# Optimization experiments

Measured on AMD Instinct MI355X. Metric: run time of the kernel, lower is better.

Reference implementation:

```python
import jax, jax.numpy as jnp
import numpy as np
from jax import lax

T, B = 64, 16
N, W, R = 256, 64, 4          # mem_slot, mem_size, read_heads
IN, OUT = 64, 64
NHID, NNOUT = 256, 256
IF_SIZE = W * R + 3 * W + 5 * R + 3  # 471
EPS = 1e-6


def setup_inputs() -> dict:
    key = jax.random.key(0)
    ks = jax.random.split(key, 8)
    in_dim = IN + R * W
    def glorot(k, shape):
        fan_in = shape[0]
        return jax.random.normal(k, shape, dtype=jnp.float32) / np.sqrt(fan_in)
    return {
        "input_data": jax.random.normal(ks[0], (T, B, IN), dtype=jnp.float32),
        "W1": glorot(ks[1], (in_dim, NHID)),
        "b1": jnp.zeros((NHID,), jnp.float32),
        "W2": glorot(ks[2], (NHID, NNOUT)),
        "b2": jnp.zeros((NNOUT,), jnp.float32),
        "W_if": glorot(ks[3], (NNOUT, IF_SIZE)),
        "b_if": jnp.zeros((IF_SIZE,), jnp.float32),
        "W_out": glorot(ks[4], (NNOUT, OUT)),
        "W_mem_out": glorot(ks[5], (R * W, OUT)),
    }


def oneplus(x):
    return 1.0 + jax.nn.softplus(x)


def content_address(mem, keys, strengths):
    # mem [B,N,W], keys [B,W,R], strengths [B,R] -> weights [B,N,R]
    mem_n = mem / (jnp.linalg.norm(mem, axis=-1, keepdims=True) + EPS)
    key_n = keys / (jnp.linalg.norm(keys, axis=1, keepdims=True) + EPS)
    sim = jnp.einsum('bnw,bwr->bnr', mem_n, key_n)
    return jax.nn.softmax(sim * strengths[:, None, :], axis=1)


def parse_interface(z):
    # z: [B, IF_SIZE] -> dict of interface components (NeuCom layout)
    o = 0
    read_keys = z[:, o:o + W * R].reshape(-1, W, R); o += W * R
    read_str = oneplus(z[:, o:o + R]); o += R
    write_key = z[:, o:o + W]; o += W
    write_str = oneplus(z[:, o:o + 1]); o += 1
    erase = jax.nn.sigmoid(z[:, o:o + W]); o += W
    write_vec = z[:, o:o + W]; o += W
    free_gates = jax.nn.sigmoid(z[:, o:o + R]); o += R
    alloc_gate = jax.nn.sigmoid(z[:, o:o + 1]); o += 1
    write_gate = jax.nn.sigmoid(z[:, o:o + 1]); o += 1
    read_modes = jax.nn.softmax(z[:, o:o + 3 * R].reshape(-1, 3, R), axis=1)
    return (read_keys, read_str, write_key, write_str, erase, write_vec,
            free_gates, alloc_gate, write_gate, read_modes)


def _dnc_forward(input_data, W1, b1, W2, b2, W_if, b_if, W_out, W_mem_out):
    Bz = input_data.shape[1]
    eye = jnp.eye(N, dtype=input_data.dtype)

    def step(carry, x_t):
        mem, usage, rw, ww, prec, link, rvec = carry
        # --- controller (feedforward) ---
        ctrl_in = jnp.concatenate([x_t, rvec.reshape(Bz, R * W)], axis=1)
        h = jnp.tanh(ctrl_in @ W1 + b1)
        nn_out = jnp.tanh(h @ W2 + b2)
        (read_keys, read_str, write_key, write_str, erase, write_vec,
         free_gates, alloc_gate, write_gate, read_modes) = parse_interface(nn_out @ W_if + b_if)
        # --- write ---
        retention = jnp.prod(1.0 - free_gates[:, None, :] * rw, axis=2)   # [B,N]
        usage = (usage + ww - usage * ww) * retention
        idx = jnp.argsort(usage, axis=1)                                  # ascending usage
        u_sorted = jnp.take_along_axis(usage, idx, axis=1)
        prod_excl = jnp.concatenate(
            [jnp.ones((Bz, 1), usage.dtype), jnp.cumprod(u_sorted, axis=1)[:, :-1]], axis=1)
        alloc_sorted = (1.0 - u_sorted) * prod_excl
        alloc = jnp.take_along_axis(alloc_sorted, jnp.argsort(idx, axis=1), axis=1)
        wc = content_address(mem, write_key[:, :, None], write_str)[:, :, 0]  # [B,N]
        ww = write_gate * (alloc_gate * alloc + (1.0 - alloc_gate) * wc)
        mem = mem * (1.0 - ww[:, :, None] * erase[:, None, :]) \
              + ww[:, :, None] * write_vec[:, None, :]
        link = (1.0 - ww[:, :, None] - ww[:, None, :]) * link \
               + ww[:, :, None] * prec[:, None, :]
        link = link * (1.0 - eye)
        prec = (1.0 - jnp.sum(ww, axis=1, keepdims=True)) * prec + ww
        # --- read ---
        rc = content_address(mem, read_keys, read_str)                    # [B,N,R]
        fwd_w = jnp.einsum('bnm,bmr->bnr', link, rw)
        bwd_w = jnp.einsum('bmn,bmr->bnr', link, rw)
        rw = (bwd_w * read_modes[:, 0][:, None, :]
              + rc * read_modes[:, 1][:, None, :]
              + fwd_w * read_modes[:, 2][:, None, :])
        rvec = jnp.einsum('bnw,bnr->bwr', mem, rw)                        # [B,W,R]
        out = nn_out @ W_out + rvec.reshape(Bz, R * W) @ W_mem_out
        view = (free_gates, alloc_gate, write_gate, rw, ww, usage)
        return (mem, usage, rw, ww, prec, link, rvec), (out, view)

    carry0 = (
        jnp.full((Bz, N, W), EPS, input_data.dtype),   # mem_mat
        jnp.zeros((Bz, N), input_data.dtype),          # usage
        jnp.zeros((Bz, N, R), input_data.dtype),       # read_weight
        jnp.zeros((Bz, N), input_data.dtype),          # write_weight
        jnp.zeros((Bz, N), input_data.dtype),          # precedence
        jnp.zeros((Bz, N, N), input_data.dtype),       # link matrix
        jnp.zeros((Bz, W, R), input_data.dtype),       # read vectors
    )
    _, (outputs, _view) = lax.scan(step, carry0, input_data)
    return outputs  # [T,B,OUT]


def reference(input_data, W1, b1, W2, b2, W_if, b_if, W_out, W_mem_out):
    return _dnc_forward(input_data, W1, b1, W2, b2, W_if, b_if, W_out, W_mem_out)
```

## Files before the change

kernel.cpp:

```cpp
#include <hip/hip_runtime.h>
#include <hip/hip_fp16.h>
#include <math.h>

#define Tt 64
#define Bb 16
#define Nn 256
#define Ww 64
#define Rr 4
#define INd 64
#define OUTd 64
#define IFS 471
#define EPSf 1e-6f

#define W1OFF   0
#define W2OFF   40960
#define WIFOFF  73728
#define WOUTOFF 134016
#define WMEMOFF 142208
#define WTOT    150400

#define LROW    129
#define LINKB   (256 * LROW * 4)
#define SCRB    16384
#define FIXF    3456
#define SMEM_MAIN (LINKB + SCRB + FIXF * 4)
#define SMEM_FB   (SCRB + FIXF * 4)

#define RWS 132

typedef _Float16 h2v __attribute__((ext_vector_type(2)));
__device__ __forceinline__ float fdot2(__half2 a, __half2 b, float c) {
    return __builtin_amdgcn_fdot2(*(h2v*)&a, *(h2v*)&b, c, false);
}
__device__ __forceinline__ __half2 pkh(float a, float b) {
    auto r = __builtin_amdgcn_cvt_pkrtz(a, b);
    return *(__half2*)&r;
}

__device__ __forceinline__ float sigm(float x) { return 1.f / (1.f + expf(-x)); }
__device__ __forceinline__ float oneplus_(float x) {
    return 1.f + fmaxf(x, 0.f) + log1pf(expf(-fabsf(x)));
}
__device__ __forceinline__ float wsum(float v) {
#pragma unroll
    for (int o = 32; o; o >>= 1) v += __shfl_xor(v, o, 64);
    return v;
}
__device__ __forceinline__ float wmaxr(float v) {
#pragma unroll
    for (int o = 32; o; o >>= 1) v = fmaxf(v, __shfl_xor(v, o, 64));
    return v;
}

__device__ __attribute__((noinline)) float gemv_part(
    const __half2* __restrict__ wP, int str, int iters,
    const __half2* __restrict__ vin)
{
    float a[8] = {0.f,0.f,0.f,0.f,0.f,0.f,0.f,0.f};
    float4 h0 = *(const float4*)(wP);
    float4 h1 = *(const float4*)(wP + str);
#pragma unroll 1
    for (int j0 = 0; j0 < iters - 8; j0 += 8) {
        int k8n = (j0 >> 2) + 2;
        float4 n0 = *(const float4*)(wP + (size_t)k8n * str);
        float4 n1 = *(const float4*)(wP + (size_t)(k8n + 1) * str);
        float4 v0 = *(const float4*)(vin + j0);
        float4 v1 = *(const float4*)(vin + j0 + 4);
        const __half2* hh0 = (const __half2*)&h0;
        const __half2* hh1 = (const __half2*)&h1;
        const __half2* vv0 = (const __half2*)&v0;
        const __half2* vv1 = (const __half2*)&v1;
#pragma unroll
        for (int u = 0; u < 4; ++u) a[u]     = fdot2(hh0[u], vv0[u], a[u]);
#pragma unroll
        for (int u = 0; u < 4; ++u) a[4 + u] = fdot2(hh1[u], vv1[u], a[4 + u]);
        h0 = n0; h1 = n1;
    }
    {
        float4 v0 = *(const float4*)(vin + iters - 8);
        float4 v1 = *(const float4*)(vin + iters - 4);
        const __half2* hh0 = (const __half2*)&h0;
        const __half2* hh1 = (const __half2*)&h1;
        const __half2* vv0 = (const __half2*)&v0;
        const __half2* vv1 = (const __half2*)&v1;
#pragma unroll
        for (int u = 0; u < 4; ++u) a[u]     = fdot2(hh0[u], vv0[u], a[u]);
#pragma unroll
        for (int u = 0; u < 4; ++u) a[4 + u] = fdot2(hh1[u], vv1[u], a[4 + u]);
    }
    return ((a[0]+a[1])+(a[2]+a[3])) + ((a[4]+a[5])+(a[6]+a[7]));
}

__global__ void convert_weights(const float* __restrict__ W1, const float* __restrict__ W2,
                                const float* __restrict__ Wif, const float* __restrict__ Wout,
                                const float* __restrict__ Wmem, __half2* __restrict__ wp) {
    int i = blockIdx.x * blockDim.x + threadIdx.x;
    if (i >= WTOT) return;
    float a, b;
    if (i < W2OFF) {
        int q = i & 3, s = i >> 2, n = s & 255, k2 = (s >> 8) * 4 + q;
        a = W1[(2*k2)*256+n];  b = W1[(2*k2+1)*256+n];
    } else if (i < WIFOFF) {
        int t = i - W2OFF;
        int q = t & 3, s = t >> 2, n = s & 255, k2 = (s >> 8) * 4 + q;
        a = W2[(2*k2)*256+n];  b = W2[(2*k2+1)*256+n];
    } else if (i < WOUTOFF) {
        int t = i - WIFOFF;
        int q = t & 3, s = t >> 2, o = s % IFS, k2 = (s / IFS) * 4 + q;
        a = Wif[(2*k2)*IFS+o]; b = Wif[(2*k2+1)*IFS+o];
    } else if (i < WMEMOFF) {
        int t = i - WOUTOFF;
        int q = t & 3, s = t >> 2, n = s & 63, k2 = (s >> 6) * 4 + q;
        a = Wout[(2*k2)*64+n]; b = Wout[(2*k2+1)*64+n];
    } else {
        int t = i - WMEMOFF;
        int q = t & 3, s = t >> 2, n = s & 63, k2 = (s >> 6) * 4 + q;
        a = Wmem[(2*k2)*64+n]; b = Wmem[(2*k2+1)*64+n];
    }
    wp[i] = __floats2half2_rn(a, b);
}

template <bool LLINK>
__global__ __launch_bounds__(1024) void dnc_kernel(
    const float* __restrict__ x, const float* __restrict__ b1,
    const float* __restrict__ b2, const float* __restrict__ bif,
    const __half2* __restrict__ wp,
    __half* __restrict__ memg,
    __half2* __restrict__ memWg,
    __half2* __restrict__ linkg,
    float* __restrict__ out)
{
    extern __shared__ __align__(16) char smem[];
    const int b = blockIdx.x;
    const int tid = threadIdx.x;
    const int lane = tid & 63;
    const int wv = tid >> 6;

    __half2* l2p = (__half2*)smem;
    __half2* gl2 = linkg + (size_t)b * (256 * LROW);
    float* scr   = (float*)(smem + (LLINK ? LINKB : 0));
    __half* scrh = (__half*)scr;
    float* fx    = (float*)((char*)scr + SCRB);

    float*   s_rw    = fx + 0;
    __half2* s_ctrlh = (__half2*)(fx + 1024);
    __half2* s_hh    = (__half2*)(fx + 1184);
    __half2* s_nnh   = (__half2*)(fx + 1312);
    __half2* s_rwh   = (__half2*)(fx + 1440);
    float* s_z     = fx + 1968;
    float* s_usage = fx + 2440;
    float* s_ww    = fx + 2696;
    float* s_prec  = fx + 2952;
    float* s_knorm = fx + 3208;
    float* s_rstr  = fx + 3212;
    float* s_rmode = fx + 3216;
    float* s_sc    = fx + 3228;
    float* s_red   = fx + 3232;
    float* s_er    = fx + 3264;
    __half2* s_keyh = (__half2*)(fx + 3328);
    float* s_srt   = scr + 1024;
    float* s_cp    = scr + 1280;
    __half2* s_keyw2 = (__half2*)(scr + 1280);
    float* s_wcdot = scr + 1536;
    float* s_wcss  = scr + 1792;
    __half2* s_wwh2 = (__half2*)(scr + 2048);
    __half2* s_tmh2 = (__half2*)(scr + 2304);

    __half*  memh  = memg + (size_t)b * (Ww * Nn);
    __half2* memh2 = (__half2*)memh;
    __half2* memW2 = memWg + (size_t)b * (32 * 256);
    __half*  memWh = (__half*)memW2;

    auto lread = [&](int idx) -> __half2 {
        if constexpr (LLINK) return l2p[idx]; else return gl2[idx];
    };
    auto lwrite = [&](int idx, __half2 v) {
        if constexpr (LLINK) l2p[idx] = v; else gl2[idx] = v;
    };

    {
        __half2 z2 = pkh(0.f, 0.f);
#pragma unroll 1
        for (int i = tid; i < 256 * LROW; i += 1024) lwrite(i, z2);
        __half2 e2 = __floats2half2_rn(EPSf, EPSf);
#pragma unroll 1
        for (int j = 0; j < 8; ++j) { memh2[tid + j * 1024] = e2; memW2[tid + j * 1024] = e2; }
        if (tid < 528) s_rwh[tid] = z2;
        if (tid < 32) {
            float2 xv = *(const float2*)&x[b * INd + 2 * tid];
            s_ctrlh[tid] = pkh(xv.x, xv.y);
        } else if (tid < 160) s_ctrlh[tid] = z2;
    }
    if (tid < 256) {
        s_usage[tid] = 0.f; s_ww[tid] = 0.f; s_prec[tid] = 0.f;
        s_rw[tid*4+0] = 0.f; s_rw[tid*4+1] = 0.f; s_rw[tid*4+2] = 0.f; s_rw[tid*4+3] = 0.f;
    }

#pragma unroll 1
    for (int t = 0; t < Tt; ++t) {
        __syncthreads();

        {
            int kc = wv >> 2, o = (wv & 3) * 64 + lane;
            scr[kc * 256 + o] = gemv_part(wp + W1OFF + o * 4 + kc * 10240, 1024, 40,
                                          s_ctrlh + kc * 40);
        }
        __syncthreads();
        if (tid < 256) {
            float v = tanhf(b1[tid] + ((scr[tid] + scr[256+tid]) + (scr[512+tid] + scr[768+tid])));
            float pv = __shfl_xor(v, 1, 64);
            if ((tid & 1) == 0) s_hh[tid >> 1] = pkh(v, pv);
        }
        __syncthreads();

        {
            int kc = wv >> 2, o = (wv & 3) * 64 + lane;
            scr[kc * 256 + o] = gemv_part(wp + W2OFF + o * 4 + kc * 8192, 1024, 32,
                                          s_hh + kc * 32);
        }
        __syncthreads();
        if (tid < 256) {
            float v = tanhf(b2[tid] + ((scr[tid] + scr[256+tid]) + (scr[512+tid] + scr[768+tid])));
            float pv = __shfl_xor(v, 1, 64);
            if ((tid & 1) == 0) s_nnh[tid >> 1] = pkh(v, pv);
        }
        __syncthreads();

        {
            int kc = wv >> 3, o = (wv & 7) * 64 + lane;
            if (o < IFS)
                scr[kc * 512 + o] = gemv_part(wp + WIFOFF + o * 4 + kc * 30144, 1884, 64,
                                              s_nnh + kc * 64);
        }
        __syncthreads();
        if (tid < IFS) {
            float v = bif[tid] + scr[tid] + scr[512 + tid];
            s_z[tid] = v;
            float pv1 = __shfl_xor(v, 1, 64);
            float pv4 = __shfl_xor(v, 4, 64);
            if (tid < 256) {
                if ((tid & 4) == 0)
                    s_keyh[(tid & 3) * 32 + (tid >> 3)] = pkh(v, pv4);
            } else if (tid >= 260 && tid < 324) {
                if ((tid & 1) == 0)
                    s_keyw2[(tid - 260) >> 1] = pkh(v, pv1);
            }
        }
        __syncthreads();

        if (wv < 4) {
            float vz = s_z[lane * 4 + wv];
            float s = wsum(vz * vz);
            if (lane == 0) s_knorm[wv] = sqrtf(s) + EPSf;
        } else if (wv == 4) {
            float vz = s_z[260 + lane];
            float s = wsum(vz * vz);
            if (lane == 0) s_sc[3] = sqrtf(s) + EPSf;
        } else if (wv == 5) {
            if (lane < 4) s_rstr[lane] = oneplus_(s_z[256 + lane]);
            else if (lane >= 8 && lane < 12) {
                int r = lane - 8;
                float a = s_z[459+r], bm = s_z[463+r], c = s_z[467+r];
                float mx = fmaxf(a, fmaxf(bm, c));
                float ea = expf(a-mx), eb = expf(bm-mx), ec = expf(c-mx);
                float inv = 1.f / ((ea+eb)+ec);
                s_rmode[0*4+r] = ea*inv; s_rmode[1*4+r] = eb*inv; s_rmode[2*4+r] = ec*inv;
            } else if (lane == 16) s_sc[0] = oneplus_(s_z[324]);
            else if (lane == 17) s_sc[1] = sigm(s_z[457]);
            else if (lane == 18) s_sc[2] = sigm(s_z[458]);
        } else if (wv == 6) {
            s_er[lane] = sigm(s_z[325 + lane]);
        } else if (wv >= 8 && wv < 12) {
            int n = tid - 512;
            float ret = 1.f;
#pragma unroll
            for (int r = 0; r < 4; ++r) {
                float fg = sigm(s_z[453 + r]);
                ret *= 1.f - fg * s_rw[n*4 + r];
            }
            float u = s_usage[n], wwo = s_ww[n];
            s_usage[n] = (u + wwo - u * wwo) * ret;
        } else if (wv >= 12) {
            int n = tid - 768;
            const __half2* mW = memW2 + n;
            float dot = 0.f, ssv = 0.f;
#pragma unroll 1
            for (int c = 0; c < 32; c += 8) {
                __half2 mv[8], kv[8];
#pragma unroll
                for (int u = 0; u < 8; ++u) mv[u] = mW[(c + u) * 256];
                *(float4*)&kv[0] = *(const float4*)(s_keyw2 + c);
                *(float4*)&kv[4] = *(const float4*)(s_keyw2 + c + 4);
#pragma unroll
                for (int u = 0; u < 8; ++u) {
                    ssv = fdot2(mv[u], mv[u], ssv);
                    dot = fdot2(mv[u], kv[u], dot);
                }
            }
            s_wcdot[n] = dot; s_wcss[n] = ssv;
        }
        __syncthreads();

        {
            int q = tid >> 8, n = tid & 255;
            float un = s_usage[n];
            float cnt = 0.f;
            int j0 = q * 64;
#pragma unroll 1
            for (int j = j0; j < j0 + 64; j += 4) {
                float4 uv = *(const float4*)&s_usage[j];
                cnt += (uv.x < un || (uv.x == un && j     < n)) ? 1.f : 0.f;
                cnt += (uv.y < un || (uv.y == un && j + 1 < n)) ? 1.f : 0.f;
                cnt += (uv.z < un || (uv.z == un && j + 2 < n)) ? 1.f : 0.f;
                cnt += (uv.w < un || (uv.w == un && j + 3 < n)) ? 1.f : 0.f;
            }
            scr[q * 256 + n] = cnt;
        }
        __syncthreads();

        if (wv == 0) {
            int rk[4]; float uu[4];
#pragma unroll
            for (int i = 0; i < 4; ++i) {
                int n = lane * 4 + i;
                float c = scr[n] + scr[256+n] + scr[512+n] + scr[768+n];
                rk[i] = (int)(c + 0.5f);
                uu[i] = s_usage[n];
                s_srt[rk[i]] = uu[i];
            }
            float4 vs = ((const float4*)s_srt)[lane];
            float p1 = vs.x * vs.y, p2 = p1 * vs.z, tot = p2 * vs.w;
            float incl = tot;
#pragma unroll
            for (int off = 1; off < 64; off <<= 1) {
                float tv = __shfl_up(incl, off, 64);
                if (lane >= off) incl *= tv;
            }
            float excl = __shfl_up(incl, 1, 64);
            if (lane == 0) excl = 1.f;
            float4 o4v; o4v.x = excl; o4v.y = excl*vs.x; o4v.z = excl*p1; o4v.w = excl*p2;
            ((float4*)s_cp)[lane] = o4v;

            float sims[4], mx = -1e30f;
#pragma unroll
            for (int i = 0; i < 4; ++i) {
                int n = lane * 4 + i;
                sims[i] = s_wcdot[n] / ((sqrtf(s_wcss[n]) + EPSf) * s_sc[3]) * s_sc[0];
                mx = fmaxf(mx, sims[i]);
            }
            mx = wmaxr(mx);
            float es[4], ls = 0.f;
#pragma unroll
            for (int i = 0; i < 4; ++i) { es[i] = expf(sims[i] - mx); ls += es[i]; }
            ls = wsum(ls);
            float ag = s_sc[1], wg = s_sc[2], inv = 1.f / ls, lw = 0.f;
#pragma unroll
            for (int i = 0; i < 4; ++i) {
                int n = lane * 4 + i;
                float alloc = (1.f - uu[i]) * s_cp[rk[i]];
                float wwn = wg * (ag * alloc + (1.f - ag) * es[i] * inv);
                s_ww[n] = wwn; lw += wwn;
                s_wwh2[n] = pkh(wwn, wwn);
                s_tmh2[n] = pkh(1.f - wwn, 1.f - wwn);
            }
            lw = wsum(lw);
            if (lane == 0) s_red[0] = lw;
        }
        __syncthreads();

        if (tid < 512) {
            int kc = tid >> 7, p = tid & 127;
            int c0 = 2 * p, c1 = c0 + 1;
            __half2 wwcp = pkh(s_ww[c0], s_ww[c1]);
            __half2 ptp  = pkh(s_prec[c0], s_prec[c1]);
            float acc[8] = {0,0,0,0,0,0,0,0};
            int kbase = kc * 64;
#pragma unroll 1
            for (int k0 = kbase; k0 < kbase + 64; k0 += 8) {
                __half2 lv[8], tm[8], wk[8];
#pragma unroll
                for (int u = 0; u < 8; ++u) lv[u] = lread((k0 + u) * LROW + p);
                *(float4*)&tm[0] = *(const float4*)(s_tmh2 + k0);
                *(float4*)&tm[4] = *(const float4*)(s_tmh2 + k0 + 4);
                *(float4*)&wk[0] = *(const float4*)(s_wwh2 + k0);
                *(float4*)&wk[4] = *(const float4*)(s_wwh2 + k0 + 4);
                __half2 ln[8];
#pragma unroll
                for (int u = 0; u < 8; ++u)
                    ln[u] = __hfma2(__hsub2(tm[u], wwcp), lv[u], __hmul2(wk[u], ptp));
#pragma unroll
                for (int u = 0; u < 8; ++u)
                    lwrite((k0 + u) * LROW + p, ln[u]);
                int kp0 = k0 >> 1;
                __half2 l0p[4], l1p[4];
#pragma unroll
                for (int i = 0; i < 4; ++i) {
                    unsigned ua = *(unsigned*)&ln[2*i], ub = *(unsigned*)&ln[2*i+1];
                    unsigned r0 = __builtin_amdgcn_perm(ub, ua, 0x05040100u);
                    unsigned r1 = __builtin_amdgcn_perm(ub, ua, 0x07060302u);
                    l0p[i] = *(__half2*)&r0; l1p[i] = *(__half2*)&r1;
                }
#pragma unroll
                for (int r = 0; r < 4; ++r) {
                    __half2 rp[4];
                    *(float4*)rp = *(const float4*)(s_rwh + r * RWS + kp0);
#pragma unroll
                    for (int i = 0; i < 4; ++i) {
                        acc[r]     = fdot2(l0p[i], rp[i], acc[r]);
                        acc[4 + r] = fdot2(l1p[i], rp[i], acc[4 + r]);
                    }
                }
            }
            if ((c0 >> 6) == kc) {
                __half2 d0 = lread(c0 * LROW + p);
                __half2 d1 = lread(c1 * LROW + p);
                float dl0 = __half2float(__low2half(d0));
                float dl1 = __half2float(__high2half(d1));
                unsigned u0 = *(unsigned*)&d0; u0 &= 0xFFFF0000u;
                unsigned u1 = *(unsigned*)&d1; u1 &= 0x0000FFFFu;
                lwrite(c0 * LROW + p, *(__half2*)&u0);
                lwrite(c1 * LROW + p, *(__half2*)&u1);
#pragma unroll
                for (int r = 0; r < 4; ++r) {
                    acc[r]     = fmaf(-dl0, s_rw[c0*4 + r], acc[r]);
                    acc[4 + r] = fmaf(-dl1, s_rw[c1*4 + r], acc[4 + r]);
                }
            }
            __half2* bp = (__half2*)scrh + (kc * 128 + p) * 4;
            bp[0] = pkh(acc[0], acc[1]);
            bp[1] = pkh(acc[2], acc[3]);
            bp[2] = pkh(acc[4], acc[5]);
            bp[3] = pkh(acc[6], acc[7]);
        } else {
            int t0 = tid - 512;
#pragma unroll 1
            for (int jb = 0; jb < 2; ++jb) {
                __half2 mv[8];
#pragma unroll
                for (int j = 0; j < 8; ++j) mv[j] = memh2[t0 + (jb * 8 + j) * 512];
#pragma unroll
                for (int j = 0; j < 8; ++j) {
                    int i2 = t0 + (jb * 8 + j) * 512;
                    int w = i2 >> 7, n2 = i2 & 127;
                    float er = s_er[w];
                    float wvv = s_z[389 + w];
                    float2 mf = __half22float2(mv[j]);
                    float wa = s_ww[2*n2], wb = s_ww[2*n2 + 1];
                    mf.x = mf.x * (1.f - wa * er) + wa * wvv;
                    mf.y = mf.y * (1.f - wb * er) + wb * wvv;
                    __half2 hv = __floats2half2_rn(mf.x, mf.y);
                    memh2[i2] = hv;
                    int wb2 = (w >> 1) * 512 + 4 * n2 + (w & 1);
                    memWh[wb2]     = __low2half(hv);
                    memWh[wb2 + 2] = __high2half(hv);
                }
            }
        }
        __syncthreads();

        {
            int q = tid >> 8, n8 = tid & 255;
            float f[4] = {0.f, 0.f, 0.f, 0.f};
            int base = n8 * LROW + q * 32;
#pragma unroll 1
            for (int j0 = 0; j0 < 32; j0 += 8) {
                __half2 lv[8];
#pragma unroll
                for (int u = 0; u < 8; ++u) lv[u] = lread(base + j0 + u);
#pragma unroll
                for (int r = 0; r < 4; ++r) {
                    __half2 rp[8];
                    *(float4*)&rp[0] = *(const float4*)(s_rwh + r * RWS + q * 32 + j0);
                    *(float4*)&rp[4] = *(const float4*)(s_rwh + r * RWS + q * 32 + j0 + 4);
#pragma unroll
                    for (int u = 0; u < 8; ++u) f[r] = fdot2(lv[u], rp[u], f[r]);
                }
            }
            __half2* fp2 = (__half2*)(scrh + 4096) + (q * 256 + n8) * 2;
            fp2[0] = pkh(f[0], f[1]);
            fp2[1] = pkh(f[2], f[3]);
            if (q == 0) s_prec[n8] = (1.f - s_red[0]) * s_prec[n8] + s_ww[n8];
        }
        __syncthreads();

        int rr = tid >> 8, n8c = tid & 255;
        float bwv = 0.f, fwv = 0.f, e_rc = 0.f;
        {
#pragma unroll
            for (int kc = 0; kc < 4; ++kc)
                bwv += __half2float(scrh[(kc * 128 + (n8c >> 1)) * 8 + (n8c & 1) * 4 + rr]);
#pragma unroll
            for (int qq = 0; qq < 4; ++qq)
                fwv += __half2float(scrh[4096 + (qq * 256 + n8c) * 4 + rr]);
            const __half2* mW = memW2 + n8c;
            const __half2* kh = s_keyh + rr * 32;
            float ssv = 0.f, dv = 0.f;
#pragma unroll 1
            for (int c = 0; c < 32; c += 8) {
                __half2 mv[8], kv[8];
#pragma unroll
                for (int u = 0; u < 8; ++u) mv[u] = mW[(c + u) * 256];
                *(float4*)&kv[0] = *(const float4*)(kh + c);
                *(float4*)&kv[4] = *(const float4*)(kh + c + 4);
#pragma unroll
                for (int u = 0; u < 8; ++u) {
                    ssv = fdot2(mv[u], mv[u], ssv);
                    dv  = fdot2(mv[u], kv[u], dv);
                }
            }
            float sim = dv / ((sqrtf(ssv) + EPSf) * s_knorm[rr]) * s_rstr[rr];
            e_rc = expf(sim);
            float s = wsum(e_rc);
            if (lane == 0) s_red[16 + wv] = s;
        }
        __syncthreads();
        {
            float sm = (s_red[16+rr*4+0] + s_red[16+rr*4+1]) + (s_red[16+rr*4+2] + s_red[16+rr*4+3]);
            float rc = e_rc / sm;
            float v = bwv * s_rmode[0*4+rr] + rc * s_rmode[1*4+rr] + fwv * s_rmode[2*4+rr];
            s_rw[n8c*4 + rr] = v;
            float pv = __shfl_xor(v, 1, 64);
            if ((n8c & 1) == 0) s_rwh[rr * RWS + (n8c >> 1)] = pkh(v, pv);
        }
        __syncthreads();

        {
            int kc = tid >> 8, o = tid & 255, w = o >> 2, r = o & 3;
            const __half2* mw2 = (const __half2*)(memh + w * 256 + kc * 64);
            const __half2* rw2 = s_rwh + r * RWS + kc * 32;
            float a = 0.f;
#pragma unroll
            for (int c = 0; c < 8; ++c) {
                __half2 mv[4], rv[4];
                *(float4*)mv = *(const float4*)(mw2 + c * 4);
                *(float4*)rv = *(const float4*)(rw2 + c * 4);
#pragma unroll
                for (int u = 0; u < 4; ++u) a = fdot2(mv[u], rv[u], a);
            }
            scr[kc * 256 + o] = a;
        }
        __syncthreads();

        if (tid < 256) {
            float v = (scr[tid] + scr[256+tid]) + (scr[512+tid] + scr[768+tid]);
            float pv = __shfl_xor(v, 1, 64);
            if ((tid & 1) == 0) s_ctrlh[32 + (tid >> 1)] = pkh(v, pv);
        } else if (tid >= 512 && tid < 544) {
            if (t + 1 < Tt) {
                int i = tid - 512;
                float2 xv = *(const float2*)&x[((t + 1) * Bb + b) * INd + 2 * i];
                s_ctrlh[i] = pkh(xv.x, xv.y);
            }
        }
        __syncthreads();

        {
            int c4 = wv, o4 = lane;
            const __half2* wsrc = (c4 < 8) ? (wp + WOUTOFF + o4 * 4 + c4 * 1024)
                                           : (wp + WMEMOFF + o4 * 4 + (c4 - 8) * 1024);
            const __half2* vsrc = (c4 < 8) ? (s_nnh + c4 * 16)
                                           : (s_ctrlh + 32 + (c4 - 8) * 16);
            scr[c4 * 64 + o4] = gemv_part(wsrc, 256, 16, vsrc);
        }
        __syncthreads();
        if (tid < 64) {
            float s = 0.f;
#pragma unroll
            for (int g = 0; g < 16; ++g) s += scr[g * 64 + tid];
            out[(t * Bb + b) * OUTd + tid] = s;
        }
    }
}

extern "C" void kernel_launch(void* const* d_in, const int* in_sizes, int n_in,
                              void* d_out, int out_size, void* d_ws, size_t ws_size,
                              hipStream_t stream) {
    const float* x    = (const float*)d_in[0];
    const float* W1   = (const float*)d_in[1];
    const float* b1   = (const float*)d_in[2];
    const float* W2   = (const float*)d_in[3];
    const float* b2   = (const float*)d_in[4];
    const float* Wif  = (const float*)d_in[5];
    const float* bif  = (const float*)d_in[6];
    const float* Wout = (const float*)d_in[7];
    const float* Wmem = (const float*)d_in[8];
    float* out = (float*)d_out;

    char* ws = (char*)d_ws;
    __half2* wp    = (__half2*)ws;
    __half*  memg  = (__half*)(ws + 601600);
    __half2* memWg = (__half2*)(ws + 601600 + 524288);
    __half2* linkg = (__half2*)(ws + 601600 + 524288 + 524288);

    convert_weights<<<dim3((WTOT + 255) / 256), dim3(256), 0, stream>>>(W1, W2, Wif, Wout, Wmem, wp);

    hipError_t rc = hipFuncSetAttribute(
        reinterpret_cast<const void*>(&dnc_kernel<true>),
        hipFuncAttributeMaxDynamicSharedMemorySize, SMEM_MAIN);
    if (rc == hipSuccess) {
        dnc_kernel<true><<<dim3(Bb), dim3(1024), SMEM_MAIN, stream>>>(
            x, b1, b2, bif, wp, memg, memWg, linkg, out);
    } else {
        dnc_kernel<false><<<dim3(Bb), dim3(1024), SMEM_FB, stream>>>(
            x, b1, b2, bif, wp, memg, memWg, linkg, out);
    }
}
```

Before: 1.837 ms.

## Use fast math intrinsics, packed sort keys, wider loads and padded link rows

Replaces tanhf, expf and divisions with __expf, clamped exp-based tanh and hardware reciprocal. It also precomputes the free-gate sigmoids once and packs usage plus index into 64-bit keys, so the allocation ranking does one integer compare per element. Other changes widen the link-matrix loads to float2 with a row pitch of 130, and unroll the content-similarity loops by 16. The cost is slightly lower accuracy in the transcendental and reciprocal ops, and more register pressure from the wider unrolls.

```diff
diff --git a/kernel.cpp b/kernel.cpp
--- a/kernel.cpp
+++ b/kernel.cpp
@@ -19,7 +19,7 @@
 #define WMEMOFF 142208
 #define WTOT    150400
 
-#define LROW    129
+#define LROW    130
 #define LINKB   (256 * LROW * 4)
 #define SCRB    16384
 #define FIXF    3456
@@ -37,7 +37,19 @@
     return *(__half2*)&r;
 }
 
-__device__ __forceinline__ float sigm(float x) { return 1.f / (1.f + expf(-x)); }
+__device__ __forceinline__ float rcpf(float x) {
+#if __has_builtin(__builtin_amdgcn_rcpf)
+    return __builtin_amdgcn_rcpf(x);
+#else
+    return 1.f / x;
+#endif
+}
+__device__ __forceinline__ float sigm(float x) { return rcpf(1.f + __expf(-x)); }
+__device__ __forceinline__ float tanh_fast(float x) {
+    float xc = fminf(fmaxf(x, -15.f), 15.f);
+    float e = __expf(2.f * xc);
+    return (e - 1.f) * rcpf(e + 1.f);
+}
 __device__ __forceinline__ float oneplus_(float x) {
     return 1.f + fmaxf(x, 0.f) + log1pf(expf(-fabsf(x)));
 }
@@ -165,6 +177,7 @@
     float* s_wcss  = scr + 1792;
     __half2* s_wwh2 = (__half2*)(scr + 2048);
     __half2* s_tmh2 = (__half2*)(scr + 2304);
+    unsigned* s_keyu = (unsigned*)(scr + 2560);
 
     __half*  memh  = memg + (size_t)b * (Ww * Nn);
     __half2* memh2 = (__half2*)memh;
@@ -176,6 +189,10 @@
     };
     auto lwrite = [&](int idx, __half2 v) {
         if constexpr (LLINK) l2p[idx] = v; else gl2[idx] = v;
+    };
+    auto lread2 = [&](int idx) -> float2 {
+        if constexpr (LLINK) return *(const float2*)(l2p + idx);
+        else return *(const float2*)(gl2 + idx);
     };
 
     {
@@ -207,7 +224,7 @@
         }
         __syncthreads();
         if (tid < 256) {
-            float v = tanhf(b1[tid] + ((scr[tid] + scr[256+tid]) + (scr[512+tid] + scr[768+tid])));
+            float v = tanh_fast(b1[tid] + ((scr[tid] + scr[256+tid]) + (scr[512+tid] + scr[768+tid])));
             float pv = __shfl_xor(v, 1, 64);
             if ((tid & 1) == 0) s_hh[tid >> 1] = pkh(v, pv);
         }
@@ -220,7 +237,7 @@
         }
         __syncthreads();
         if (tid < 256) {
-            float v = tanhf(b2[tid] + ((scr[tid] + scr[256+tid]) + (scr[512+tid] + scr[768+tid])));
+            float v = tanh_fast(b2[tid] + ((scr[tid] + scr[256+tid]) + (scr[512+tid] + scr[768+tid])));
             float pv = __shfl_xor(v, 1, 64);
             if ((tid & 1) == 0) s_nnh[tid >> 1] = pkh(v, pv);
         }
@@ -244,6 +261,8 @@
             } else if (tid >= 260 && tid < 324) {
                 if ((tid & 1) == 0)
                     s_keyw2[(tid - 260) >> 1] = pkh(v, pv1);
+            } else if (tid >= 453 && tid < 457) {
+                s_red[8 + (tid - 453)] = sigm(v);
             }
         }
         __syncthreads();
@@ -262,8 +281,8 @@
                 int r = lane - 8;
                 float a = s_z[459+r], bm = s_z[463+r], c = s_z[467+r];
                 float mx = fmaxf(a, fmaxf(bm, c));
-                float ea = expf(a-mx), eb = expf(bm-mx), ec = expf(c-mx);
-                float inv = 1.f / ((ea+eb)+ec);
+                float ea = __expf(a-mx), eb = __expf(bm-mx), ec = __expf(c-mx);
+                float inv = rcpf((ea+eb)+ec);
                 s_rmode[0*4+r] = ea*inv; s_rmode[1*4+r] = eb*inv; s_rmode[2*4+r] = ec*inv;
             } else if (lane == 16) s_sc[0] = oneplus_(s_z[324]);
             else if (lane == 17) s_sc[1] = sigm(s_z[457]);
@@ -272,27 +291,31 @@
             s_er[lane] = sigm(s_z[325 + lane]);
         } else if (wv >= 8 && wv < 12) {
             int n = tid - 512;
-            float ret = 1.f;
-#pragma unroll
-            for (int r = 0; r < 4; ++r) {
-                float fg = sigm(s_z[453 + r]);
-                ret *= 1.f - fg * s_rw[n*4 + r];
-            }
+            float4 rw4 = *(const float4*)&s_rw[n*4];
+            float4 fg4 = *(const float4*)&s_red[8];
+            float ret = (1.f - fg4.x*rw4.x) * (1.f - fg4.y*rw4.y)
+                      * (1.f - fg4.z*rw4.z) * (1.f - fg4.w*rw4.w);
             float u = s_usage[n], wwo = s_ww[n];
-            s_usage[n] = (u + wwo - u * wwo) * ret;
+            float unew = (u + wwo - u * wwo) * ret;
+            s_usage[n] = unew;
+            unsigned ub = __float_as_uint(unew);
+            s_keyu[2*n]     = (ub << 8) | (unsigned)n;
+            s_keyu[2*n + 1] = ub >> 24;
         } else if (wv >= 12) {
             int n = tid - 768;
             const __half2* mW = memW2 + n;
             float dot = 0.f, ssv = 0.f;
 #pragma unroll 1
-            for (int c = 0; c < 32; c += 8) {
-                __half2 mv[8], kv[8];
-#pragma unroll
-                for (int u = 0; u < 8; ++u) mv[u] = mW[(c + u) * 256];
-                *(float4*)&kv[0] = *(const float4*)(s_keyw2 + c);
-                *(float4*)&kv[4] = *(const float4*)(s_keyw2 + c + 4);
-#pragma unroll
-                for (int u = 0; u < 8; ++u) {
+            for (int hf = 0; hf < 2; ++hf) {
+                __half2 mv[16], kv[16];
+#pragma unroll
+                for (int u = 0; u < 16; ++u) mv[u] = mW[(hf * 16 + u) * 256];
+                *(float4*)&kv[0]  = *(const float4*)(s_keyw2 + hf*16);
+                *(float4*)&kv[4]  = *(const float4*)(s_keyw2 + hf*16 + 4);
+                *(float4*)&kv[8]  = *(const float4*)(s_keyw2 + hf*16 + 8);
+                *(float4*)&kv[12] = *(const float4*)(s_keyw2 + hf*16 + 12);
+#pragma unroll
+                for (int u = 0; u < 16; ++u) {
                     ssv = fdot2(mv[u], mv[u], ssv);
                     dot = fdot2(mv[u], kv[u], dot);
                 }
@@ -303,18 +326,17 @@
 
         {
             int q = tid >> 8, n = tid & 255;
-            float un = s_usage[n];
-            float cnt = 0.f;
+            unsigned long long kn = *(const unsigned long long*)&s_keyu[2*n];
+            int cnt = 0;
+            const unsigned long long* kp = (const unsigned long long*)s_keyu;
             int j0 = q * 64;
-#pragma unroll 1
-            for (int j = j0; j < j0 + 64; j += 4) {
-                float4 uv = *(const float4*)&s_usage[j];
-                cnt += (uv.x < un || (uv.x == un && j     < n)) ? 1.f : 0.f;
-                cnt += (uv.y < un || (uv.y == un && j + 1 < n)) ? 1.f : 0.f;
-                cnt += (uv.z < un || (uv.z == un && j + 2 < n)) ? 1.f : 0.f;
-                cnt += (uv.w < un || (uv.w == un && j + 3 < n)) ? 1.f : 0.f;
-            }
-            scr[q * 256 + n] = cnt;
+#pragma unroll 8
+            for (int j = j0; j < j0 + 64; j += 2) {
+                ulonglong2 kk = *(const ulonglong2*)&kp[j];
+                cnt += (kk.x < kn);
+                cnt += (kk.y < kn);
+            }
+            scr[q * 256 + n] = (float)cnt;
         }
         __syncthreads();
 
@@ -351,9 +373,9 @@
             mx = wmaxr(mx);
             float es[4], ls = 0.f;
 #pragma unroll
-            for (int i = 0; i < 4; ++i) { es[i] = expf(sims[i] - mx); ls += es[i]; }
+            for (int i = 0; i < 4; ++i) { es[i] = __expf(sims[i] - mx); ls += es[i]; }
             ls = wsum(ls);
-            float ag = s_sc[1], wg = s_sc[2], inv = 1.f / ls, lw = 0.f;
+            float ag = s_sc[1], wg = s_sc[2], inv = rcpf(ls), lw = 0.f;
 #pragma unroll
             for (int i = 0; i < 4; ++i) {
                 int n = lane * 4 + i;
@@ -465,8 +487,12 @@
 #pragma unroll 1
             for (int j0 = 0; j0 < 32; j0 += 8) {
                 __half2 lv[8];
-#pragma unroll
-                for (int u = 0; u < 8; ++u) lv[u] = lread(base + j0 + u);
+                float2 a0 = lread2(base + j0);
+                float2 a1 = lread2(base + j0 + 2);
+                float2 a2 = lread2(base + j0 + 4);
+                float2 a3 = lread2(base + j0 + 6);
+                *(float2*)&lv[0] = a0; *(float2*)&lv[2] = a1;
+                *(float2*)&lv[4] = a2; *(float2*)&lv[6] = a3;
 #pragma unroll
                 for (int r = 0; r < 4; ++r) {
                     __half2 rp[8];
@@ -496,27 +522,29 @@
             const __half2* kh = s_keyh + rr * 32;
             float ssv = 0.f, dv = 0.f;
 #pragma unroll 1
-            for (int c = 0; c < 32; c += 8) {
-                __half2 mv[8], kv[8];
-#pragma unroll
-                for (int u = 0; u < 8; ++u) mv[u] = mW[(c + u) * 256];
-                *(float4*)&kv[0] = *(const float4*)(kh + c);
-                *(float4*)&kv[4] = *(const float4*)(kh + c + 4);
-#pragma unroll
-                for (int u = 0; u < 8; ++u) {
+            for (int hf = 0; hf < 2; ++hf) {
+                __half2 mv[16], kv[16];
+#pragma unroll
+                for (int u = 0; u < 16; ++u) mv[u] = mW[(hf * 16 + u) * 256];
+                *(float4*)&kv[0]  = *(const float4*)(kh + hf*16);
+                *(float4*)&kv[4]  = *(const float4*)(kh + hf*16 + 4);
+                *(float4*)&kv[8]  = *(const float4*)(kh + hf*16 + 8);
+                *(float4*)&kv[12] = *(const float4*)(kh + hf*16 + 12);
+#pragma unroll
+                for (int u = 0; u < 16; ++u) {
                     ssv = fdot2(mv[u], mv[u], ssv);
                     dv  = fdot2(mv[u], kv[u], dv);
                 }
             }
             float sim = dv / ((sqrtf(ssv) + EPSf) * s_knorm[rr]) * s_rstr[rr];
-            e_rc = expf(sim);
+            e_rc = __expf(sim);
             float s = wsum(e_rc);
             if (lane == 0) s_red[16 + wv] = s;
         }
         __syncthreads();
         {
             float sm = (s_red[16+rr*4+0] + s_red[16+rr*4+1]) + (s_red[16+rr*4+2] + s_red[16+rr*4+3]);
-            float rc = e_rc / sm;
+            float rc = e_rc * rcpf(sm);
             float v = bwv * s_rmode[0*4+rr] + rc * s_rmode[1*4+rr] + fwv * s_rmode[2*4+rr];
             s_rw[n8c*4 + rr] = v;
             float pv = __shfl_xor(v, 1, 64);
```

New measurement: 1.680 ms. 8.5% less time.
